# Optimization experiments

Hardware: AMD Instinct MI355X
Metric: run time of the kernel (lower is better)

## Reference

```python
import jax, jax.numpy as jnp
import numpy as np

W = 512
ITERS = 10
CELL_W = 200.0 / W
EPS = 1e-10


def relu(x):
    return jnp.maximum(x, 0.0)


def simple_gradient(t, noise):
    # t: [B,W,W], noise: [1,W,W] (broadcasts over batch). Matches torch version exactly,
    # including the 1.1*x - x boundary rows/cols.
    dx = 0.5 * jnp.concatenate([t[:, :1, :] * 1.1 - t[:, :1, :],
                                t[:, 2:, :] - t[:, :-2, :],
                                t[:, -1:, :] * 0.9 - t[:, -1:, :]], axis=1)
    dy = 0.5 * jnp.concatenate([t[:, :, :1] * 1.1 - t[:, :, :1],
                                t[:, :, 2:] - t[:, :, :-2],
                                t[:, :, -1:] * 0.9 - t[:, :, -1:]], axis=2)
    mag = jnp.sqrt(dx * dx + dy * dy + EPS / 10)
    rX = noise
    rY = jnp.sqrt(1.0 - rX * rX)
    factor = relu(EPS - mag)
    fdx = (dx + factor * rX) / (mag + factor)
    fdy = (dy + factor * rY) / (mag + factor)
    return jnp.stack([fdx, fdy], axis=-1)  # [B,W,W,2]


def bilinear_sample(t, offset):
    # Equivalent of F.grid_sample on (t-1) with mode='bilinear', padding_mode='zeros',
    # align_corners=True, then +1. coord_grid[0,row,col] = [col, row] (identity grid),
    # so x samples along the last (col) axis, y along the row axis.
    col = jnp.arange(W, dtype=t.dtype)[None, None, :]
    row = jnp.arange(W, dtype=t.dtype)[None, :, None]
    fx = col + offset[..., 0]  # [B,W,W]
    fy = row + offset[..., 1]
    x0 = jnp.floor(fx)
    y0 = jnp.floor(fy)
    wx1 = fx - x0
    wy1 = fy - y0
    tm1 = t - 1.0

    def gather(ix, iy):
        valid = (ix >= 0) & (ix <= W - 1) & (iy >= 0) & (iy <= W - 1)
        ixc = jnp.clip(ix, 0, W - 1).astype(jnp.int32)
        iyc = jnp.clip(iy, 0, W - 1).astype(jnp.int32)
        v = jax.vmap(lambda im, r, c: im[r, c])(tm1, iyc, ixc)
        return jnp.where(valid, v, 0.0)

    out = ((1 - wy1) * ((1 - wx1) * gather(x0, y0) + wx1 * gather(x0 + 1, y0))
           + wy1 * ((1 - wx1) * gather(x0, y0 + 1) + wx1 * gather(x0 + 1, y0 + 1)))
    return out + 1.0


def displace(a, delta):
    # Faithful to the torch displace: post_x is computed then DISCARDED (the original
    # passes `a`, not post_x, into the y pass and returns post_y), so only the y pass
    # affects the output and we skip the dead x pass.
    dy = delta[..., 1]
    t1 = relu(-dy) * a
    t2 = relu(1.0 - jnp.abs(dy)) * a
    t3 = relu(dy) * a
    t1 = t1.at[:, :, -1].set(0.0)  # zero last col (offset_axis=2 branch)
    t3 = t3.at[:, :, 0].set(0.0)   # zero first col
    return t1 + t2 + t3


def reference(input_terrain, random_rainfall, random_gradient, rain_rate,
              evaporation_rate, min_height_delta, height_epsilon, gravity,
              sediment_capacity_constant, dissolving_rate, deposition_rate):
    B = input_terrain.shape[0]
    terrain = ((1.0 - input_terrain) / 2.0).reshape(B, W, W)
    zeros = jnp.zeros((B, W, W), dtype=terrain.dtype)

    def step(carry, noises):
        terrain, sediment, water, velocity = carry
        rain, gnoise = noises  # each [W,W]
        water = water + relu(rain_rate) * rain
        gradient = simple_gradient(terrain, gnoise[None])
        neighbor = bilinear_sample(terrain, -gradient)
        hd = terrain - neighbor
        hds = jnp.sign(relu(hd - height_epsilon))
        nhd = hds * jnp.maximum(hd, min_height_delta)
        sed_cap = nhd / CELL_W * velocity * water * relu(sediment_capacity_constant)
        ftb = relu(jnp.sign(-hd))
        first = jnp.minimum(relu(-hd), sediment)
        sdiff = sediment - sed_cap
        third = (1.0 - ftb) * (relu(sdiff * deposition_rate) - relu(-sdiff * dissolving_rate))
        dep = jnp.maximum(-relu(hd), first + third)
        sediment = sediment - dep
        terrain = terrain + dep
        sediment = displace(sediment, gradient)
        water = displace(water, gradient)
        velocity = relu(gravity) * hd / CELL_W
        water = water * (1.0 - relu(evaporation_rate))
        return (terrain, sediment, water, velocity), None

    noises = (random_rainfall[0], random_gradient[0])  # [ITERS,W,W] each
    (terrain, _, _, _), _ = jax.lax.scan(step, (terrain, zeros, zeros, zeros), noises)
    terrain = terrain[:, None]  # [B,1,W,W]
    return relu(1.0 + (1.0 - terrain * 2.0)) - 1.0


def setup_inputs() -> dict:
    key = jax.random.key(0)
    k1, k2, k3 = jax.random.split(key, 3)
    B = 16
    cell_area = CELL_W ** 2
    return {
        "input_terrain": jax.random.normal(k1, (B, 1, W, W), dtype=jnp.float32),
        "random_rainfall": jax.random.uniform(k2, (1, ITERS, W, W), dtype=jnp.float32),
        "random_gradient": jax.random.uniform(k3, (1, ITERS, W, W), dtype=jnp.float32),
        "rain_rate": jnp.array([0.1 * cell_area], dtype=jnp.float32),
        "evaporation_rate": jnp.array([0.02], dtype=jnp.float32),
        "min_height_delta": jnp.array([0.05], dtype=jnp.float32),
        "height_epsilon": jnp.array([0.001], dtype=jnp.float32),
        "gravity": jnp.array([50.0], dtype=jnp.float32),
        "sediment_capacity_constant": jnp.array([15.0], dtype=jnp.float32),
        "dissolving_rate": jnp.array([0.1], dtype=jnp.float32),
        "deposition_rate": jnp.array([0.0025], dtype=jnp.float32),
    }
```

## Files before the change

### kernel.cpp

```cpp
#include <hip/hip_runtime.h>

#pragma clang fp contract(off)

constexpr int WW   = 512;
constexpr int NPIX = WW * WW;
constexpr int NTOT = 16 * NPIX;
constexpr int HH   = 8;
constexpr int AR   = 16;
constexpr int BR   = 12;
constexpr int NBLK = 16 * (WW / HH);

__device__ __forceinline__ void cell_math(
    const float* __restrict__ lds, int rowOfs, int r, int c,
    float rain_v, float gno_v,
    float rr, float evapr, float minhd, float heps, float gravr, float sccr,
    float diss, float depo,
    float& s_io, float& w_io, float& v_io, float& t_out, bool fin)
{
    #pragma clang fp contract(off)
    const float CELLW = 0.390625f;

    float t_c = lds[(r - rowOfs) * WW + c];

    float w = fmaf(rr, rain_v, w_io);

    float dx, dy;
    if      (r == 0)      dx = 0.5f * fmaf(t_c, 1.1f, -t_c);
    else if (r == WW - 1) dx = 0.5f * fmaf(t_c, 0.9f, -t_c);
    else dx = 0.5f * (lds[(r + 1 - rowOfs) * WW + c] - lds[(r - 1 - rowOfs) * WW + c]);
    if      (c == 0)      dy = 0.5f * fmaf(t_c, 1.1f, -t_c);
    else if (c == WW - 1) dy = 0.5f * fmaf(t_c, 0.9f, -t_c);
    else dy = 0.5f * (lds[(r - rowOfs) * WW + c + 1] - lds[(r - rowOfs) * WW + c - 1]);

    float mag = sqrtf(fmaf(dx, dx, dy * dy) + 1e-11f);
    float fdx = dx / mag;
    float fdy = dy / mag;

    float fx  = (float)c + (-fdx);
    float fy  = (float)r + (-fdy);
    float x0f = floorf(fx), y0f = floorf(fy);
    float wx1 = fx - x0f;
    float wy1 = fy - y0f;
    int x0 = (int)x0f, y0 = (int)y0f;
    int x1 = x0 + 1,   y1 = y0 + 1;

    bool vx0 = (x0 >= 0) & (x0 < WW);
    bool vx1 = (x1 >= 0) & (x1 < WW);
    bool vy0 = (y0 >= 0) & (y0 < WW);
    bool vy1 = (y1 >= 0) & (y1 < WW);
    int x0c = min(max(x0, 0), WW - 1), x1c = min(max(x1, 0), WW - 1);
    int y0c = min(max(y0, 0), WW - 1), y1c = min(max(y1, 0), WW - 1);
    int ty0 = y0c - rowOfs, ty1 = y1c - rowOfs;

    float g00 = (vx0 && vy0) ? (lds[ty0 * WW + x0c] - 1.0f) : 0.0f;
    float g10 = (vx1 && vy0) ? (lds[ty0 * WW + x1c] - 1.0f) : 0.0f;
    float g01 = (vx0 && vy1) ? (lds[ty1 * WW + x0c] - 1.0f) : 0.0f;
    float g11 = (vx1 && vy1) ? (lds[ty1 * WW + x1c] - 1.0f) : 0.0f;

    float wx0 = 1.0f - wx1;
    float wy0 = 1.0f - wy1;
    float rowA = fmaf(wx0, g00, wx1 * g10);
    float rowB = fmaf(wx0, g01, wx1 * g11);
    float bil  = fmaf(wy0, rowA, wy1 * rowB);
    float neighbor = bil + 1.0f;

    float hd = t_c - neighbor;

    float v = v_io;
    float s = s_io;

    float hds  = ((hd - heps) > 0.0f) ? 1.0f : 0.0f;
    float nhd  = hds * fmaxf(hd, minhd);
    float q1 = nhd / CELLW;
    float q2 = q1 * v;
    float q3 = q2 * w;
    float sdiff = fmaf(-q3, sccr, s);
    float ftb   = (hd < 0.0f) ? 1.0f : 0.0f;
    float first = fminf(fmaxf(-hd, 0.0f), s);
    float ra = fmaxf(sdiff * depo, 0.0f);
    float rb = fmaxf((-sdiff) * diss, 0.0f);
    float deparg = fmaf(1.0f - ftb, ra - rb, first);
    float dep    = fmaxf(-fmaxf(hd, 0.0f), deparg);

    float s_new = s - dep;
    float t_new = t_c + dep;

    float rn = fmaxf(-fdy, 0.0f);
    float rm = fmaxf(1.0f - fabsf(fdy), 0.0f);
    float rp = fmaxf(fdy, 0.0f);

    float s1 = (c == WW - 1) ? 0.0f : rn * s_new;
    float s3 = (c == 0)      ? 0.0f : rp * s_new;
    s_io = fmaf(rm, s_new, s1) + s3;

    float w1 = (c == WW - 1) ? 0.0f : rn * w;
    float w3 = (c == 0)      ? 0.0f : rp * w;
    float wd = fmaf(rm, w, w1) + w3;
    w_io = wd * (1.0f - evapr);

    v_io = (gravr * hd) / CELLW;

    if (fin) {
        float aa = fmaf(-t_new, 2.0f, 1.0f);
        float bq = 1.0f + aa;
        t_out = fmaxf(bq, 0.0f) - 1.0f;
    } else {
        t_out = t_new;
    }
}

template <bool FIRST, bool FINAL>
__global__ __launch_bounds__(512, 6) void erosion_fused(
    const float* __restrict__ tin, float* __restrict__ tout,
    const float* __restrict__ sed_in, const float* __restrict__ wat_in,
    const float* __restrict__ vel_in,
    float* __restrict__ sed_out, float* __restrict__ wat_out,
    float* __restrict__ vel_out,
    const float* __restrict__ rain0, const float* __restrict__ gno0,
    const float* __restrict__ rain1, const float* __restrict__ gno1,
    const float* __restrict__ s_rain_rate, const float* __restrict__ s_evap,
    const float* __restrict__ s_minhd, const float* __restrict__ s_heps,
    const float* __restrict__ s_grav, const float* __restrict__ s_scc,
    const float* __restrict__ s_diss, const float* __restrict__ s_depo)
{
    #pragma clang fp contract(off)
    __shared__ float A[AR * WW];

    const int c   = threadIdx.x;
    const int img = blockIdx.x >> 6;
    const int r0  = (blockIdx.x & 63) * HH;
    const float* tb = tin + (size_t)img * NPIX;
    const int gbase = img * NPIX + c;

    float rr    = fmaxf(s_rain_rate[0], 0.0f);
    float evapr = fmaxf(s_evap[0], 0.0f);
    float minhd = s_minhd[0];
    float heps  = s_heps[0];
    float gravr = fmaxf(s_grav[0], 0.0f);
    float sccr  = fmaxf(s_scc[0], 0.0f);
    float diss  = s_diss[0];
    float depo  = s_depo[0];

    {
        const int rg = c >> 7;
        const int c4 = (c & 127) << 2;
        #pragma unroll
        for (int j = 0; j < 4; ++j) {
            int ridx = j * 4 + rg;
            int y = r0 - 4 + ridx;
            if (y >= 0 && y < WW) {
                float4 v = *reinterpret_cast<const float4*>(tb + y * WW + c4);
                if (FIRST) {
                    v.x = (1.0f - v.x) / 2.0f;
                    v.y = (1.0f - v.y) / 2.0f;
                    v.z = (1.0f - v.z) / 2.0f;
                    v.w = (1.0f - v.w) / 2.0f;
                }
                *reinterpret_cast<float4*>(&A[ridx * WW + c4]) = v;
            }
        }
    }
    __syncthreads();

    float sK[HH], wK[HH], vK[HH];
    #pragma unroll
    for (int i = 0; i < BR; ++i) {
        const int x = r0 - 2 + i;
        const bool live1 = (x >= 0) && (x < WW);
        float s0 = 0.0f, w0 = 0.0f, v0 = 0.0f, tn = 0.0f;
        if (live1) {
            if (!FIRST) {
                int g = gbase + x * WW;
                s0 = sed_in[g]; w0 = wat_in[g]; v0 = vel_in[g];
            }
            cell_math(A, r0 - 4, x, c, rain0[x * WW + c], gno0[x * WW + c],
                      rr, evapr, minhd, heps, gravr, sccr, diss, depo,
                      s0, w0, v0, tn, false);
        }
        __syncthreads();
        if (live1) {
            A[i * WW + c] = tn;
            if (i >= 2 && i <= HH + 1) {
                sK[i - 2] = s0; wK[i - 2] = w0; vK[i - 2] = v0;
            }
        }
        __syncthreads();
        if (i >= 4) {
            const int j  = i - 4;
            const int x2 = r0 + j;
            float s2 = sK[j], w2 = wK[j], v2 = vK[j];
            float tn2;
            cell_math(A, r0 - 2, x2, c, rain1[x2 * WW + c], gno1[x2 * WW + c],
                      rr, evapr, minhd, heps, gravr, sccr, diss, depo,
                      s2, w2, v2, tn2, FINAL);
            int g = gbase + x2 * WW;
            tout[g] = tn2;
            if (!FINAL) { sed_out[g] = s2; wat_out[g] = w2; vel_out[g] = v2; }
        }
    }
}

extern "C" void kernel_launch(void* const* d_in, const int* in_sizes, int n_in,
                              void* d_out, int out_size, void* d_ws, size_t ws_size,
                              hipStream_t stream) {
    const float* in_terr    = (const float*)d_in[0];
    const float* rain_all   = (const float*)d_in[1];
    const float* gnoise_all = (const float*)d_in[2];
    const float* p_rr       = (const float*)d_in[3];
    const float* p_evap     = (const float*)d_in[4];
    const float* p_minhd    = (const float*)d_in[5];
    const float* p_heps     = (const float*)d_in[6];
    const float* p_grav     = (const float*)d_in[7];
    const float* p_scc      = (const float*)d_in[8];
    const float* p_diss     = (const float*)d_in[9];
    const float* p_depo     = (const float*)d_in[10];

    float* T0  = (float*)d_out;
    float* ws  = (float*)d_ws;
    float* T1  = ws;
    float* T2  = ws + (size_t)NTOT;
    float* sA  = ws + (size_t)2 * NTOT;
    float* wA  = ws + (size_t)3 * NTOT;
    float* vA  = ws + (size_t)4 * NTOT;
    float* sB, * wB, * vB;
    if (ws_size >= (size_t)8 * NTOT * sizeof(float)) {
        sB = ws + (size_t)5 * NTOT;
        wB = ws + (size_t)6 * NTOT;
        vB = ws + (size_t)7 * NTOT;
    } else {
        sB = sA; wB = wA; vB = vA;
    }

    dim3 grid(NBLK), block(512);
    #define RN(k) (rain_all   + (size_t)(k) * NPIX)
    #define GN(k) (gnoise_all + (size_t)(k) * NPIX)
    #define SCAL p_rr, p_evap, p_minhd, p_heps, p_grav, p_scc, p_diss, p_depo

    erosion_fused<true, false><<<grid, block, 0, stream>>>(
        in_terr, T1, sA, wA, vA, sA, wA, vA, RN(0), GN(0), RN(1), GN(1), SCAL);
    erosion_fused<false, false><<<grid, block, 0, stream>>>(
        T1, T2, sA, wA, vA, sB, wB, vB, RN(2), GN(2), RN(3), GN(3), SCAL);
    erosion_fused<false, false><<<grid, block, 0, stream>>>(
        T2, T1, sB, wB, vB, sA, wA, vA, RN(4), GN(4), RN(5), GN(5), SCAL);
    erosion_fused<false, false><<<grid, block, 0, stream>>>(
        T1, T2, sA, wA, vA, sB, wB, vB, RN(6), GN(6), RN(7), GN(7), SCAL);
    erosion_fused<false, true><<<grid, block, 0, stream>>>(
        T2, T0, sB, wB, vB, sA, wA, vA, RN(8), GN(8), RN(9), GN(9), SCAL);

    #undef RN
    #undef GN
    #undef SCAL
}
```

Measured before the change: 303.6 us.

## Fuse five erosion launches into one cooperative kernel with grid syncs

Replaces the five back-to-back kernel launches with a single cooperative persistent kernel. It loops over the five double-step groups and uses a grid-wide sync between them, falling back to separate launches when cooperative launch or occupancy is insufficient. It also delays the second-stage row computation by one row so that one __syncthreads per loop iteration can be dropped, and adds a tail step to handle the last row. This targets launch gaps and block-level barrier cost, at the price of a grid barrier and a residency requirement of at least 4 blocks per CU.

```diff
diff --git a/kernel.cpp b/kernel.cpp
--- a/kernel.cpp
+++ b/kernel.cpp
@@ -1,4 +1,7 @@
 #include <hip/hip_runtime.h>
+#include <hip/hip_cooperative_groups.h>
+
+namespace cg = cooperative_groups;
 
 #pragma clang fp contract(off)
 
@@ -109,37 +112,21 @@
     }
 }
 
-template <bool FIRST, bool FINAL>
-__global__ __launch_bounds__(512, 6) void erosion_fused(
-    const float* __restrict__ tin, float* __restrict__ tout,
+__device__ __forceinline__ void run_group(
+    bool FIRST, bool FINAL,
+    const float* __restrict__ tb,
+    float* __restrict__ tout,
     const float* __restrict__ sed_in, const float* __restrict__ wat_in,
     const float* __restrict__ vel_in,
     float* __restrict__ sed_out, float* __restrict__ wat_out,
     float* __restrict__ vel_out,
     const float* __restrict__ rain0, const float* __restrict__ gno0,
     const float* __restrict__ rain1, const float* __restrict__ gno1,
-    const float* __restrict__ s_rain_rate, const float* __restrict__ s_evap,
-    const float* __restrict__ s_minhd, const float* __restrict__ s_heps,
-    const float* __restrict__ s_grav, const float* __restrict__ s_scc,
-    const float* __restrict__ s_diss, const float* __restrict__ s_depo)
+    float rr, float evapr, float minhd, float heps, float gravr, float sccr,
+    float diss, float depo,
+    int img, int r0, int c, float* __restrict__ A)
 {
-    #pragma clang fp contract(off)
-    __shared__ float A[AR * WW];
-
-    const int c   = threadIdx.x;
-    const int img = blockIdx.x >> 6;
-    const int r0  = (blockIdx.x & 63) * HH;
-    const float* tb = tin + (size_t)img * NPIX;
     const int gbase = img * NPIX + c;
-
-    float rr    = fmaxf(s_rain_rate[0], 0.0f);
-    float evapr = fmaxf(s_evap[0], 0.0f);
-    float minhd = s_minhd[0];
-    float heps  = s_heps[0];
-    float gravr = fmaxf(s_grav[0], 0.0f);
-    float sccr  = fmaxf(s_scc[0], 0.0f);
-    float diss  = s_diss[0];
-    float depo  = s_depo[0];
 
     {
         const int rg = c >> 7;
@@ -184,9 +171,8 @@
                 sK[i - 2] = s0; wK[i - 2] = w0; vK[i - 2] = v0;
             }
         }
-        __syncthreads();
-        if (i >= 4) {
-            const int j  = i - 4;
+        if (i >= 5) {
+            const int j  = i - 5;
             const int x2 = r0 + j;
             float s2 = sK[j], w2 = wK[j], v2 = vK[j];
             float tn2;
@@ -197,6 +183,116 @@
             tout[g] = tn2;
             if (!FINAL) { sed_out[g] = s2; wat_out[g] = w2; vel_out[g] = v2; }
         }
+    }
+    __syncthreads();
+
+    {
+        const int j  = HH - 1;
+        const int x2 = r0 + j;
+        float s2 = sK[j], w2 = wK[j], v2 = vK[j];
+        float tn2;
+        cell_math(A, r0 - 2, x2, c, rain1[x2 * WW + c], gno1[x2 * WW + c],
+                  rr, evapr, minhd, heps, gravr, sccr, diss, depo,
+                  s2, w2, v2, tn2, FINAL);
+        int g = gbase + x2 * WW;
+        tout[g] = tn2;
+        if (!FINAL) { sed_out[g] = s2; wat_out[g] = w2; vel_out[g] = v2; }
+    }
+}
+
+template <bool FIRST, bool FINAL>
+__global__ __launch_bounds__(512, 6) void erosion_step(
+    const float* __restrict__ tin, float* __restrict__ tout,
+    const float* __restrict__ sed_in, const float* __restrict__ wat_in,
+    const float* __restrict__ vel_in,
+    float* __restrict__ sed_out, float* __restrict__ wat_out,
+    float* __restrict__ vel_out,
+    const float* __restrict__ rain0, const float* __restrict__ gno0,
+    const float* __restrict__ rain1, const float* __restrict__ gno1,
+    const float* __restrict__ s_rain_rate, const float* __restrict__ s_evap,
+    const float* __restrict__ s_minhd, const float* __restrict__ s_heps,
+    const float* __restrict__ s_grav, const float* __restrict__ s_scc,
+    const float* __restrict__ s_diss, const float* __restrict__ s_depo)
+{
+    #pragma clang fp contract(off)
+    __shared__ float A[AR * WW];
+    const int c   = threadIdx.x;
+    const int img = blockIdx.x >> 6;
+    const int r0  = (blockIdx.x & 63) * HH;
+
+    float rr    = fmaxf(s_rain_rate[0], 0.0f);
+    float evapr = fmaxf(s_evap[0], 0.0f);
+    float minhd = s_minhd[0];
+    float heps  = s_heps[0];
+    float gravr = fmaxf(s_grav[0], 0.0f);
+    float sccr  = fmaxf(s_scc[0], 0.0f);
+    float diss  = s_diss[0];
+    float depo  = s_depo[0];
+
+    run_group(FIRST, FINAL, tin + (size_t)img * NPIX, tout,
+              sed_in, wat_in, vel_in, sed_out, wat_out, vel_out,
+              rain0, gno0, rain1, gno1,
+              rr, evapr, minhd, heps, gravr, sccr, diss, depo,
+              img, r0, c, A);
+}
+
+__global__ __launch_bounds__(512, 6) void erosion_coop(
+    const float* __restrict__ tin0, float* __restrict__ T0,
+    float* __restrict__ T1, float* __restrict__ T2,
+    float* __restrict__ sA, float* __restrict__ wA, float* __restrict__ vA,
+    float* __restrict__ sB, float* __restrict__ wB, float* __restrict__ vB,
+    const float* __restrict__ rain_all, const float* __restrict__ gno_all,
+    const float* __restrict__ s_rain_rate, const float* __restrict__ s_evap,
+    const float* __restrict__ s_minhd, const float* __restrict__ s_heps,
+    const float* __restrict__ s_grav, const float* __restrict__ s_scc,
+    const float* __restrict__ s_diss, const float* __restrict__ s_depo)
+{
+    #pragma clang fp contract(off)
+    __shared__ float A[AR * WW];
+    cg::grid_group grid = cg::this_grid();
+
+    const int c   = threadIdx.x;
+    const int img = blockIdx.x >> 6;
+    const int r0  = (blockIdx.x & 63) * HH;
+
+    float rr    = fmaxf(s_rain_rate[0], 0.0f);
+    float evapr = fmaxf(s_evap[0], 0.0f);
+    float minhd = s_minhd[0];
+    float heps  = s_heps[0];
+    float gravr = fmaxf(s_grav[0], 0.0f);
+    float sccr  = fmaxf(s_scc[0], 0.0f);
+    float diss  = s_diss[0];
+    float depo  = s_depo[0];
+
+    #pragma unroll 1
+    for (int g = 0; g < 5; ++g) {
+        const bool FIRST = (g == 0), FINAL = (g == 4);
+        const float* tin; float* tout;
+        if      (g == 0) { tin = tin0; tout = T1; }
+        else if (g == 1) { tin = T1;   tout = T2; }
+        else if (g == 2) { tin = T2;   tout = T1; }
+        else if (g == 3) { tin = T1;   tout = T2; }
+        else             { tin = T2;   tout = T0; }
+        const bool inB  = (g == 2) || (g == 4);
+        const bool outB = (g == 1) || (g == 3);
+        const float* sin_ = inB ? sB : sA;
+        const float* win_ = inB ? wB : wA;
+        const float* vin_ = inB ? vB : vA;
+        float* sout_ = outB ? sB : sA;
+        float* wout_ = outB ? wB : wA;
+        float* vout_ = outB ? vB : vA;
+        const float* rain0 = rain_all + (size_t)(2 * g) * NPIX;
+        const float* gno0  = gno_all  + (size_t)(2 * g) * NPIX;
+        const float* rain1 = rain_all + (size_t)(2 * g + 1) * NPIX;
+        const float* gno1  = gno_all  + (size_t)(2 * g + 1) * NPIX;
+
+        run_group(FIRST, FINAL, tin + (size_t)img * NPIX, tout,
+                  sin_, win_, vin_, sout_, wout_, vout_,
+                  rain0, gno0, rain1, gno1,
+                  rr, evapr, minhd, heps, gravr, sccr, diss, depo,
+                  img, r0, c, A);
+
+        if (g < 4) grid.sync();
     }
 }
 
@@ -222,13 +318,40 @@
     float* sA  = ws + (size_t)2 * NTOT;
     float* wA  = ws + (size_t)3 * NTOT;
     float* vA  = ws + (size_t)4 * NTOT;
-    float* sB, * wB, * vB;
-    if (ws_size >= (size_t)8 * NTOT * sizeof(float)) {
-        sB = ws + (size_t)5 * NTOT;
-        wB = ws + (size_t)6 * NTOT;
-        vB = ws + (size_t)7 * NTOT;
-    } else {
-        sB = sA; wB = wA; vB = vA;
+    const bool haveB = ws_size >= (size_t)8 * NTOT * sizeof(float);
+    float* sB = haveB ? ws + (size_t)5 * NTOT : sA;
+    float* wB = haveB ? ws + (size_t)6 * NTOT : wA;
+    float* vB = haveB ? ws + (size_t)7 * NTOT : vA;
+
+    static int s_coop_attr = -1;
+    if (s_coop_attr < 0) {
+        int dev = 0;
+        hipGetDevice(&dev);
+        int v = 0;
+        hipDeviceGetAttribute(&v, hipDeviceAttributeCooperativeLaunch, dev);
+        s_coop_attr = v ? 1 : 0;
+    }
+    static int s_maxB = -1;
+    if (s_maxB < 0) {
+        int mb = 0;
+        hipError_t e = hipOccupancyMaxActiveBlocksPerMultiprocessor(
+            &mb, erosion_coop, 512, 0);
+        s_maxB = (e == hipSuccess) ? mb : 0;
+    }
+    const bool coop_ok = haveB && s_coop_attr == 1 && s_maxB >= 4;
+
+    if (coop_ok) {
+        void* args[] = {
+            (void*)&in_terr, (void*)&T0, (void*)&T1, (void*)&T2,
+            (void*)&sA, (void*)&wA, (void*)&vA,
+            (void*)&sB, (void*)&wB, (void*)&vB,
+            (void*)&rain_all, (void*)&gnoise_all,
+            (void*)&p_rr, (void*)&p_evap, (void*)&p_minhd, (void*)&p_heps,
+            (void*)&p_grav, (void*)&p_scc, (void*)&p_diss, (void*)&p_depo,
+        };
+        hipLaunchCooperativeKernel(erosion_coop, dim3(NBLK), dim3(512),
+                                   args, 0, stream);
+        return;
     }
 
     dim3 grid(NBLK), block(512);
@@ -236,15 +359,15 @@
     #define GN(k) (gnoise_all + (size_t)(k) * NPIX)
     #define SCAL p_rr, p_evap, p_minhd, p_heps, p_grav, p_scc, p_diss, p_depo
 
-    erosion_fused<true, false><<<grid, block, 0, stream>>>(
+    erosion_step<true, false><<<grid, block, 0, stream>>>(
         in_terr, T1, sA, wA, vA, sA, wA, vA, RN(0), GN(0), RN(1), GN(1), SCAL);
-    erosion_fused<false, false><<<grid, block, 0, stream>>>(
+    erosion_step<false, false><<<grid, block, 0, stream>>>(
         T1, T2, sA, wA, vA, sB, wB, vB, RN(2), GN(2), RN(3), GN(3), SCAL);
-    erosion_fused<false, false><<<grid, block, 0, stream>>>(
+    erosion_step<false, false><<<grid, block, 0, stream>>>(
         T2, T1, sB, wB, vB, sA, wA, vA, RN(4), GN(4), RN(5), GN(5), SCAL);
-    erosion_fused<false, false><<<grid, block, 0, stream>>>(
+    erosion_step<false, false><<<grid, block, 0, stream>>>(
         T1, T2, sA, wA, vA, sB, wB, vB, RN(6), GN(6), RN(7), GN(7), SCAL);
-    erosion_fused<false, true><<<grid, block, 0, stream>>>(
+    erosion_step<false, true><<<grid, block, 0, stream>>>(
         T2, T0, sB, wB, vB, sA, wA, vA, RN(8), GN(8), RN(9), GN(9), SCAL);
 
     #undef RN
```

New measurement: 301.8 us. Within noise of the previous version (-0.6%).
